# Kernel tuning notes

Measured on AMD Instinct MI355X. Metric: run time of the kernel, lower is better.

The kernel has to match this reference:

```python
import jax, jax.numpy as jnp
import numpy as np
import math
from jax import lax

C = 128
K = 9
PAD = K // 2


def conv1d(x, w, b):
    # x: [B, C, L], w: [C_out, C_in, K], b: [C_out]
    y = lax.conv_general_dilated(x, w, window_strides=(1,), padding=[(PAD, PAD)],
                                 dimension_numbers=('NCH', 'OIH', 'NCH'))
    return y + b[None, :, None]


def _scan_fwd(slices, w, b):
    # slices: [S, B, C, L]; recurrence s_i = s_i + relu(conv(s_{i-1})) for i=1..S-1
    def step(carry, s):
        new = s + jax.nn.relu(conv1d(carry, w, b))
        return new, new
    _, out = lax.scan(step, slices[0], slices[1:])
    return jnp.concatenate([slices[:1], out], axis=0)


def _scan_bwd(slices, w, b):
    # recurrence s_i = s_i + relu(conv(s_{i+1})) for i=S-2..1 (endpoints untouched)
    def step(carry, s):
        new = s + jax.nn.relu(conv1d(carry, w, b))
        return new, new
    seg = jnp.flip(slices[1:-1], axis=0)
    _, out = lax.scan(step, slices[-1], seg)
    return jnp.concatenate([slices[:1], jnp.flip(out, axis=0), slices[-1:]], axis=0)


def setup_inputs() -> dict:
    key = jax.random.key(0)
    ks = jax.random.split(key, 9)
    B, H, W = 64, 36, 100
    bound = math.sqrt(2.0 / (C * K * 5))
    bias_bound = 1.0 / math.sqrt(C * K)
    x = jax.random.normal(ks[0], (B, C, H, W), dtype=jnp.float32)
    def wgt(k):
        return jax.random.uniform(k, (C, C, K), dtype=jnp.float32, minval=-bound, maxval=bound)
    def bia(k):
        return jax.random.uniform(k, (C,), dtype=jnp.float32, minval=-bias_bound, maxval=bias_bound)
    return {
        'x': x,
        'w_d': wgt(ks[1]), 'b_d': bia(ks[2]),
        'w_u': wgt(ks[3]), 'b_u': bia(ks[4]),
        'w_r': wgt(ks[5]), 'b_r': bia(ks[6]),
        'w_l': wgt(ks[7]), 'b_l': bia(ks[8]),
    }


def reference(x, w_d, b_d, w_u, b_u, w_r, b_r, w_l, b_l):
    # Down then up passes: recurrence over H, 1D conv along W.
    rows = jnp.moveaxis(x, 2, 0)            # [H, B, C, W]
    rows = _scan_fwd(rows, w_d, b_d)
    rows = _scan_bwd(rows, w_u, b_u)
    y = jnp.moveaxis(rows, 0, 2)            # [B, C, H, W]
    # Right then left passes: recurrence over W, 1D conv along H.
    cols = jnp.moveaxis(y, 3, 0)            # [W, B, C, H]
    cols = _scan_fwd(cols, w_r, b_r)
    cols = _scan_bwd(cols, w_l, b_l)
    return jnp.moveaxis(cols, 0, 3)         # [B, C, H, W]
```

## Files before the change

kernel.cpp:

```cpp
#include <hip/hip_runtime.h>

#define B_ 64
#define C_ 128
#define H_ 36
#define W_ 100
#define K_ 9
#define PAD_ 4
#define NCHUNK 36
#define LDSTRIDE 152
#define NR_H 120
#define NR_W 56
#define PASSSZ (8 * NCHUNK * 64 * 8)
#define FBT_ELEMS ((size_t)B_ * W_ * C_ * H_)
#define FBT_OFF ((size_t)4 << 20)

typedef __attribute__((ext_vector_type(8))) short short8;
typedef __attribute__((ext_vector_type(4))) float f32x4;
typedef unsigned short u16;

__device__ __forceinline__ u16 f2bf(float f) {
    union { float f; unsigned u; } v; v.f = f;
    unsigned u = v.u;
    return (u16)((u + 0x7fffu + ((u >> 16) & 1u)) >> 16);
}
__device__ __forceinline__ float bf2f(u16 h) {
    union { unsigned u; float f; } v; v.u = ((unsigned)h) << 16; return v.f;
}
__device__ __forceinline__ float lodv(const float* p) { return *p; }
__device__ __forceinline__ float lodv(const u16* p) { return bf2f(*p); }
__device__ __forceinline__ void storv(float* p, float v) { *p = v; }
__device__ __forceinline__ void storv(u16* p, float v) { *p = f2bf(v); }

__global__ void prep_kernel(const float* __restrict__ wd, const float* __restrict__ wu,
                            const float* __restrict__ wr, const float* __restrict__ wl,
                            u16* __restrict__ afrag) {
    const int bid = blockIdx.x;
    const int p = bid / (8 * NCHUNK);
    const int rem = bid % (8 * NCHUNK);
    const int ct = rem / NCHUNK;
    const int kk = rem % NCHUNK;
    const float* w = (p == 0) ? wd : (p == 1) ? wu : (p == 2) ? wr : wl;
    const int lane = threadIdx.x;
    const int co = ct * 16 + (lane & 15);
    const int k0 = kk * 32 + ((lane >> 4) << 3);
    u16 v[8];
#pragma unroll
    for (int j = 0; j < 8; ++j) {
        const int k = k0 + j;
        const int kw = k >> 7;
        const int ci = k & 127;
        v[j] = f2bf(w[(co * C_ + ci) * K_ + kw]);
    }
    u16* dst = afrag + ((size_t)(bid * 64 + lane)) * 8;
#pragma unroll
    for (int j = 0; j < 8; ++j) dst[j] = v[j];
}

__device__ __forceinline__ void step_barrier() {
    asm volatile("s_waitcnt lgkmcnt(0)\n\ts_barrier" ::: "memory");
}

template <int AXIS, bool SKIP_T, bool STORE_T, int NROWS, typename TF>
__device__ __forceinline__ void run_pass(
    const float* __restrict__ stbase,
    const float* __restrict__ sread,
    float* __restrict__ fb,
    TF* __restrict__ fbT,
    const u16* __restrict__ afr,
    const float* __restrict__ bias,
    const int nsteps, const int start, const int dir, const int stage_t,
    u16* __restrict__ lds)
{
    constexpr int L = (AXIS == 0) ? W_ : H_;
    constexpr int NLT = (AXIS == 0) ? 7 : 3;
    const int tid = threadIdx.x;
    const int lane = tid & 63;
    const int wv = tid >> 6;
    const int q = lane >> 4, r = lane & 15;
    const int ct0 = 2 * wv, ct1 = ct0 + 1;
    const int cob0 = ct0 * 16 + (q << 2);
    const int cob1 = ct1 * 16 + (q << 2);

    short8 areg0[NCHUNK], areg1[NCHUNK];
    {
        const u16* ap0 = afr + ((size_t)(ct0 * NCHUNK) * 64 + lane) * 8;
        const u16* ap1 = afr + ((size_t)(ct1 * NCHUNK) * 64 + lane) * 8;
#pragma unroll
        for (int kk = 0; kk < NCHUNK; ++kk) {
            areg0[kk] = *(const short8*)(ap0 + (size_t)kk * 512);
            areg1[kk] = *(const short8*)(ap1 + (size_t)kk * 512);
            asm("" : "+a"(areg1[kk]));
            if (kk >= 18) asm("" : "+a"(areg0[kk]));
        }
    }
    float bias0[4], bias1[4];
#pragma unroll
    for (int j = 0; j < 4; ++j) { bias0[j] = bias[cob0 + j]; bias1[j] = bias[cob1 + j]; }

    __syncthreads();

    for (int e = tid; e < C_ * L; e += 256) {
        const int c = e / L, l = e - c * L;
        float fv;
        if constexpr (SKIP_T)
            fv = lodv(&fbT[((size_t)stage_t * C_ + c) * H_ + l]);
        else
            fv = stbase[(AXIS == 0) ? (c * H_ + stage_t) * W_ + l
                                    : (c * H_ + l) * W_ + stage_t];
        lds[(l + PAD_) * LDSTRIDE + c] = f2bf(fv);
        if constexpr (STORE_T && !SKIP_T)
            storv(&fbT[((size_t)stage_t * C_ + c) * H_ + l], fv);
    }
    __syncthreads();

    for (int s = 1; s <= nsteps; ++s) {
        const int cur = (s - 1) & 1, nxt = s & 1;
        const int t = start + dir * s;
        const u16* curb = lds + (size_t)cur * NROWS * LDSTRIDE;
        u16* nxtb = lds + (size_t)nxt * NROWS * LDSTRIDE;

#pragma unroll
        for (int ltp = 0; ltp < NLT; ltp += 2) {
            const bool two = (ltp + 1 < NLT);
            const int lA = ltp * 16 + r;
            const int lB = lA + 16;
            const bool vA = (lA < L);
            const bool vB = two && (lB < L);

            auto ld_skip = [&](int co, int l) -> float {
                if constexpr (SKIP_T) {
                    return lodv(&fbT[((size_t)t * C_ + co) * H_ + l]);
                } else {
                    const int fi = (AXIS == 0) ? (co * H_ + t) * W_ + l
                                               : (co * H_ + l) * W_ + t;
                    return sread[fi];
                }
            };
            float svA0[4], svA1[4], svB0[4], svB1[4];
#pragma unroll
            for (int j = 0; j < 4; ++j) {
                svA0[j] = vA ? ld_skip(cob0 + j, lA) : 0.0f;
                svA1[j] = vA ? ld_skip(cob1 + j, lA) : 0.0f;
                if (two) {
                    svB0[j] = vB ? ld_skip(cob0 + j, lB) : 0.0f;
                    svB1[j] = vB ? ld_skip(cob1 + j, lB) : 0.0f;
                }
            }

            f32x4 aA0 = {bias0[0], bias0[1], bias0[2], bias0[3]};
            f32x4 aA1 = {bias1[0], bias1[1], bias1[2], bias1[3]};
            f32x4 aB0 = aA0;
            f32x4 aB1 = aA1;
#pragma unroll
            for (int kk = 0; kk < NCHUNK; ++kk) {
                const int kw = kk >> 2;
                const int cib = ((kk & 3) << 5) | (q << 3);
                const short8 bvA = *(const short8*)&curb[(lA + kw) * LDSTRIDE + cib];
                aA0 = __builtin_amdgcn_mfma_f32_16x16x32_bf16(areg0[kk], bvA, aA0, 0, 0, 0);
                aA1 = __builtin_amdgcn_mfma_f32_16x16x32_bf16(areg1[kk], bvA, aA1, 0, 0, 0);
                if (two) {
                    const short8 bvB = *(const short8*)&curb[(lB + kw) * LDSTRIDE + cib];
                    aB0 = __builtin_amdgcn_mfma_f32_16x16x32_bf16(areg0[kk], bvB, aB0, 0, 0, 0);
                    aB1 = __builtin_amdgcn_mfma_f32_16x16x32_bf16(areg1[kk], bvB, aB1, 0, 0, 0);
                }
            }

            auto epi = [&](int l, bool valid, const f32x4& a, const float* sv,
                           const int cob) {
                if (!valid) return;
                union { u16 s4[4]; unsigned long long v; } pk;
#pragma unroll
                for (int j = 0; j < 4; ++j) {
                    const float conv = fmaxf(a[j], 0.0f);
                    const float nv = sv[j] + conv;
                    if constexpr (STORE_T) {
                        storv(&fbT[((size_t)t * C_ + cob + j) * H_ + l], nv);
                    } else {
                        const int fi = (AXIS == 0) ? ((cob + j) * H_ + t) * W_ + l
                                                   : ((cob + j) * H_ + l) * W_ + t;
                        fb[fi] = nv;
                    }
                    pk.s4[j] = f2bf(nv);
                }
                *(unsigned long long*)&nxtb[(l + PAD_) * LDSTRIDE + cob] = pk.v;
            };
            epi(lA, vA, aA0, svA0, cob0);
            epi(lA, vA, aA1, svA1, cob1);
            if (two) {
                epi(lB, vB, aB0, svB0, cob0);
                epi(lB, vB, aB1, svB1, cob1);
            }
        }
        step_barrier();
    }
}

__global__ __launch_bounds__(256, 1) void spatialH(
    const float* __restrict__ x, float* __restrict__ fb,
    const u16* __restrict__ afrag,
    const float* __restrict__ bd, const float* __restrict__ bu) {
    __shared__ __align__(16) u16 lds[2 * NR_H * LDSTRIDE];
    const int b = blockIdx.x;
    const int tid = threadIdx.x;
    const float* xb = x + (size_t)b * C_ * H_ * W_;
    float* fbb = fb + (size_t)b * C_ * H_ * W_;

    for (int e = tid; e < C_ * W_; e += 256) {
        const int c = e / W_, w = e - c * W_;
        fbb[(c * H_) * W_ + w] = xb[(c * H_) * W_ + w];
    }
    for (int off = tid * 8; off < 2 * NR_H * LDSTRIDE; off += 256 * 8)
        *(uint4*)(&lds[off]) = make_uint4(0u, 0u, 0u, 0u);

    run_pass<0, false, false, NR_H, float>(xb, xb, fbb, (float*)nullptr,
        afrag + (size_t)0 * PASSSZ, bd, 35, 0, +1, 0, lds);
    run_pass<0, false, false, NR_H, float>(fbb, fbb, fbb, (float*)nullptr,
        afrag + (size_t)1 * PASSSZ, bu, 34, 35, -1, 35, lds);
}

template <typename TF>
__global__ void t1_kernel(const float* __restrict__ in, TF* __restrict__ fbT) {
    __shared__ float tile[16 * 36 * 17];
    const int tid = threadIdx.x;
    const int bid = blockIdx.x;
    const int b = bid / 56;
    const int rem = bid % 56;
    const int cs = rem / 7, wc = rem % 7;
    const int w0 = wc * 16;
    const int wlen = (w0 + 16 <= W_) ? 16 : (W_ - w0);
    const int c0 = cs * 16;
    const float* src = in + (size_t)b * C_ * H_ * W_;
    TF* dst = fbT + (size_t)b * W_ * C_ * H_;

    for (int j = tid; j < 576 * 16; j += 256) {
        const int w = j & 15;
        const int ch = j >> 4;
        if (w >= wlen) continue;
        const int c = ch / 36, h = ch - c * 36;
        tile[(c * 36 + h) * 17 + w] = src[((size_t)(c0 + c) * H_ + h) * W_ + w0 + w];
    }
    __syncthreads();
    for (int i = tid; i < 576 * wlen; i += 256) {
        const int w = i / 576;
        const int ch = i - w * 576;
        const int c = ch / 36, h = ch - c * 36;
        storv(&dst[((size_t)(w0 + w) * C_ + c0 + c) * H_ + h],
              tile[(c * 36 + h) * 17 + w]);
    }
}

template <typename TF>
__global__ __launch_bounds__(256, 1) void spatialW(
    TF* __restrict__ fbT, const u16* __restrict__ afrag,
    const float* __restrict__ br_, const float* __restrict__ bl_) {
    __shared__ __align__(16) u16 lds[2 * NR_W * LDSTRIDE];
    const int b = blockIdx.x;
    const int tid = threadIdx.x;
    TF* fbTb = fbT + (size_t)b * W_ * C_ * H_;

    for (int off = tid * 8; off < 2 * NR_W * LDSTRIDE; off += 256 * 8)
        *(uint4*)(&lds[off]) = make_uint4(0u, 0u, 0u, 0u);

    run_pass<1, true, true, NR_W, TF>((const float*)nullptr, (const float*)nullptr,
        (float*)nullptr, fbTb, afrag + (size_t)2 * PASSSZ, br_, 99, 0, +1, 0, lds);
    run_pass<1, true, true, NR_W, TF>((const float*)nullptr, (const float*)nullptr,
        (float*)nullptr, fbTb, afrag + (size_t)3 * PASSSZ, bl_, 98, 99, -1, 99, lds);
}

template <typename TF>
__global__ void t2_kernel(const TF* __restrict__ fbT, float* __restrict__ out) {
    __shared__ float tile[16 * 36 * 17];
    const int tid = threadIdx.x;
    const int bid = blockIdx.x;
    const int b = bid / 56;
    const int rem = bid % 56;
    const int cs = rem / 7, wc = rem % 7;
    const int w0 = wc * 16;
    const int wlen = (w0 + 16 <= W_) ? 16 : (W_ - w0);
    const int c0 = cs * 16;
    const TF* src = fbT + (size_t)b * W_ * C_ * H_;

    for (int i = tid; i < 576 * wlen; i += 256) {
        const int w = i / 576;
        const int ch = i - w * 576;
        const int c = ch / 36, h = ch - c * 36;
        tile[(c * 36 + h) * 17 + w] = lodv(&src[((size_t)(w0 + w) * C_ + c0 + c) * H_ + h]);
    }
    __syncthreads();
    for (int j = tid; j < 576 * 16; j += 256) {
        const int w = j & 15;
        const int ch = j >> 4;
        if (w >= wlen) continue;
        const int c = ch / 36, h = ch - c * 36;
        out[(((size_t)b * C_ + c0 + c) * H_ + h) * W_ + w0 + w] = tile[(c * 36 + h) * 17 + w];
    }
}

extern "C" void kernel_launch(void* const* d_in, const int* in_sizes, int n_in,
                              void* d_out, int out_size, void* d_ws, size_t ws_size,
                              hipStream_t stream) {
    const float* x  = (const float*)d_in[0];
    const float* wd = (const float*)d_in[1];
    const float* bd = (const float*)d_in[2];
    const float* wu = (const float*)d_in[3];
    const float* bu = (const float*)d_in[4];
    const float* wr = (const float*)d_in[5];
    const float* br = (const float*)d_in[6];
    const float* wl = (const float*)d_in[7];
    const float* bl = (const float*)d_in[8];

    u16* afrag = (u16*)((char*)d_ws + 1024);
    void* fbTp = (char*)d_ws + FBT_OFF;
    const bool f32ok = ws_size >= FBT_OFF + sizeof(float) * FBT_ELEMS;

    prep_kernel<<<dim3(4 * 8 * NCHUNK), dim3(64), 0, stream>>>(wd, wu, wr, wl, afrag);
    spatialH<<<dim3(64), dim3(256), 0, stream>>>(x, (float*)d_out, afrag, bd, bu);
    if (f32ok) {
        t1_kernel<float><<<dim3(64 * 56), dim3(256), 0, stream>>>(
            (const float*)d_out, (float*)fbTp);
        spatialW<float><<<dim3(64), dim3(256), 0, stream>>>(
            (float*)fbTp, afrag, br, bl);
        t2_kernel<float><<<dim3(64 * 56), dim3(256), 0, stream>>>(
            (const float*)fbTp, (float*)d_out);
    } else {
        t1_kernel<u16><<<dim3(64 * 56), dim3(256), 0, stream>>>(
            (const float*)d_out, (u16*)fbTp);
        spatialW<u16><<<dim3(64), dim3(256), 0, stream>>>(
            (u16*)fbTp, afrag, br, bl);
        t2_kernel<u16><<<dim3(64 * 56), dim3(256), 0, stream>>>(
            (const u16*)fbTp, (float*)d_out);
    }
}
```

Measured before the change: 1.465 ms.

## Reuse LDS B-fragments across conv taps via DPP lane shifts

The step loop is restructured so every L-tile's B fragment is loaded from LDS once per channel quarter, and later kernel taps are produced by DPP row shifts across lanes that pull in the next tile's data, instead of issuing a separate LDS read for each of the nine taps. All L-tiles' accumulators are kept live together, and the skip loads are hoisted ahead of the MMA loop. This cuts LDS read traffic by roughly nine times but raises VGPR pressure, so more A fragments are pinned to AGPRs. The DPP row_shr with bound_ctrl and the OR-merge of the neighbour tile must reproduce the padded window exactly at the 16-lane row edges.

```diff
diff --git a/kernel.cpp b/kernel.cpp
--- a/kernel.cpp
+++ b/kernel.cpp
@@ -16,7 +16,10 @@
 
 typedef __attribute__((ext_vector_type(8))) short short8;
 typedef __attribute__((ext_vector_type(4))) float f32x4;
+typedef __attribute__((ext_vector_type(4))) int i32x4;
 typedef unsigned short u16;
+
+union fragU { short8 s; i32x4 i; };
 
 __device__ __forceinline__ u16 f2bf(float f) {
     union { float f; unsigned u; } v; v.f = f;
@@ -30,6 +33,22 @@
 __device__ __forceinline__ float lodv(const u16* p) { return bf2f(*p); }
 __device__ __forceinline__ void storv(float* p, float v) { *p = v; }
 __device__ __forceinline__ void storv(u16* p, float v) { *p = f2bf(v); }
+
+__device__ __forceinline__ i32x4 dpp_shift(i32x4 cur, i32x4 nxt) {
+    i32x4 o;
+#pragma unroll
+    for (int j = 0; j < 4; ++j)
+        o[j] = __builtin_amdgcn_update_dpp(0, cur[j], 0x101, 0xF, 0xF, false)
+             | __builtin_amdgcn_update_dpp(0, nxt[j], 0x11F, 0xF, 0xF, false);
+    return o;
+}
+__device__ __forceinline__ i32x4 dpp_shift_last(i32x4 cur) {
+    i32x4 o;
+#pragma unroll
+    for (int j = 0; j < 4; ++j)
+        o[j] = __builtin_amdgcn_update_dpp(0, cur[j], 0x101, 0xF, 0xF, false);
+    return o;
+}
 
 __global__ void prep_kernel(const float* __restrict__ wd, const float* __restrict__ wu,
                             const float* __restrict__ wr, const float* __restrict__ wl,
@@ -90,7 +109,7 @@
             areg0[kk] = *(const short8*)(ap0 + (size_t)kk * 512);
             areg1[kk] = *(const short8*)(ap1 + (size_t)kk * 512);
             asm("" : "+a"(areg1[kk]));
-            if (kk >= 18) asm("" : "+a"(areg0[kk]));
+            if (kk >= 9) asm("" : "+a"(areg0[kk]));
         }
     }
     float bias0[4], bias1[4];
@@ -119,76 +138,82 @@
         const u16* curb = lds + (size_t)cur * NROWS * LDSTRIDE;
         u16* nxtb = lds + (size_t)nxt * NROWS * LDSTRIDE;
 
-#pragma unroll
-        for (int ltp = 0; ltp < NLT; ltp += 2) {
-            const bool two = (ltp + 1 < NLT);
-            const int lA = ltp * 16 + r;
-            const int lB = lA + 16;
-            const bool vA = (lA < L);
-            const bool vB = two && (lB < L);
-
-            auto ld_skip = [&](int co, int l) -> float {
-                if constexpr (SKIP_T) {
-                    return lodv(&fbT[((size_t)t * C_ + co) * H_ + l]);
+        auto ld_skip = [&](int co, int l) -> float {
+            if constexpr (SKIP_T) {
+                return lodv(&fbT[((size_t)t * C_ + co) * H_ + l]);
+            } else {
+                const int fi = (AXIS == 0) ? (co * H_ + t) * W_ + l
+                                           : (co * H_ + l) * W_ + t;
+                return sread[fi];
+            }
+        };
+
+        float sv0[NLT][4], sv1[NLT][4];
+#pragma unroll
+        for (int lt = 0; lt < NLT; ++lt) {
+            const int l = lt * 16 + r;
+            const bool v = (l < L);
+#pragma unroll
+            for (int j = 0; j < 4; ++j) {
+                sv0[lt][j] = v ? ld_skip(cob0 + j, l) : 0.0f;
+                sv1[lt][j] = v ? ld_skip(cob1 + j, l) : 0.0f;
+            }
+        }
+
+        f32x4 acc0[NLT], acc1[NLT];
+#pragma unroll
+        for (int lt = 0; lt < NLT; ++lt) {
+            acc0[lt] = f32x4{bias0[0], bias0[1], bias0[2], bias0[3]};
+            acc1[lt] = f32x4{bias1[0], bias1[1], bias1[2], bias1[3]};
+        }
+
+#pragma unroll
+        for (int cq = 0; cq < 4; ++cq) {
+            i32x4 frag[NLT];
+#pragma unroll
+            for (int lt = 0; lt < NLT; ++lt)
+                frag[lt] = *(const i32x4*)&curb[(lt * 16 + r) * LDSTRIDE + (cq << 5) + (q << 3)];
+#pragma unroll
+            for (int kw = 0; kw < 9; ++kw) {
+                const int kk = kw * 4 + cq;
+#pragma unroll
+                for (int lt = 0; lt < NLT; ++lt) {
+                    fragU u; u.i = frag[lt];
+                    acc0[lt] = __builtin_amdgcn_mfma_f32_16x16x32_bf16(areg0[kk], u.s, acc0[lt], 0, 0, 0);
+                    acc1[lt] = __builtin_amdgcn_mfma_f32_16x16x32_bf16(areg1[kk], u.s, acc1[lt], 0, 0, 0);
+                }
+                if (kw < 8) {
+#pragma unroll
+                    for (int lt = 0; lt < NLT; ++lt)
+                        frag[lt] = (lt + 1 < NLT) ? dpp_shift(frag[lt], frag[lt + 1])
+                                                  : dpp_shift_last(frag[lt]);
+                }
+            }
+        }
+
+        auto epi = [&](int l, const f32x4& a, const float* sv, const int cob) {
+            union { u16 s4[4]; unsigned long long v; } pk;
+#pragma unroll
+            for (int j = 0; j < 4; ++j) {
+                const float conv = fmaxf(a[j], 0.0f);
+                const float nv = sv[j] + conv;
+                if constexpr (STORE_T) {
+                    storv(&fbT[((size_t)t * C_ + cob + j) * H_ + l], nv);
                 } else {
-                    const int fi = (AXIS == 0) ? (co * H_ + t) * W_ + l
-                                               : (co * H_ + l) * W_ + t;
-                    return sread[fi];
+                    const int fi = (AXIS == 0) ? ((cob + j) * H_ + t) * W_ + l
+                                               : ((cob + j) * H_ + l) * W_ + t;
+                    fb[fi] = nv;
                 }
-            };
-            float svA0[4], svA1[4], svB0[4], svB1[4];
-#pragma unroll
-            for (int j = 0; j < 4; ++j) {
-                svA0[j] = vA ? ld_skip(cob0 + j, lA) : 0.0f;
-                svA1[j] = vA ? ld_skip(cob1 + j, lA) : 0.0f;
-                if (two) {
-                    svB0[j] = vB ? ld_skip(cob0 + j, lB) : 0.0f;
-                    svB1[j] = vB ? ld_skip(cob1 + j, lB) : 0.0f;
-                }
-            }
-
-            f32x4 aA0 = {bias0[0], bias0[1], bias0[2], bias0[3]};
-            f32x4 aA1 = {bias1[0], bias1[1], bias1[2], bias1[3]};
-            f32x4 aB0 = aA0;
-            f32x4 aB1 = aA1;
-#pragma unroll
-            for (int kk = 0; kk < NCHUNK; ++kk) {
-                const int kw = kk >> 2;
-                const int cib = ((kk & 3) << 5) | (q << 3);
-                const short8 bvA = *(const short8*)&curb[(lA + kw) * LDSTRIDE + cib];
-                aA0 = __builtin_amdgcn_mfma_f32_16x16x32_bf16(areg0[kk], bvA, aA0, 0, 0, 0);
-                aA1 = __builtin_amdgcn_mfma_f32_16x16x32_bf16(areg1[kk], bvA, aA1, 0, 0, 0);
-                if (two) {
-                    const short8 bvB = *(const short8*)&curb[(lB + kw) * LDSTRIDE + cib];
-                    aB0 = __builtin_amdgcn_mfma_f32_16x16x32_bf16(areg0[kk], bvB, aB0, 0, 0, 0);
-                    aB1 = __builtin_amdgcn_mfma_f32_16x16x32_bf16(areg1[kk], bvB, aB1, 0, 0, 0);
-                }
-            }
-
-            auto epi = [&](int l, bool valid, const f32x4& a, const float* sv,
-                           const int cob) {
-                if (!valid) return;
-                union { u16 s4[4]; unsigned long long v; } pk;
-#pragma unroll
-                for (int j = 0; j < 4; ++j) {
-                    const float conv = fmaxf(a[j], 0.0f);
-                    const float nv = sv[j] + conv;
-                    if constexpr (STORE_T) {
-                        storv(&fbT[((size_t)t * C_ + cob + j) * H_ + l], nv);
-                    } else {
-                        const int fi = (AXIS == 0) ? ((cob + j) * H_ + t) * W_ + l
-                                                   : ((cob + j) * H_ + l) * W_ + t;
-                        fb[fi] = nv;
-                    }
-                    pk.s4[j] = f2bf(nv);
-                }
-                *(unsigned long long*)&nxtb[(l + PAD_) * LDSTRIDE + cob] = pk.v;
-            };
-            epi(lA, vA, aA0, svA0, cob0);
-            epi(lA, vA, aA1, svA1, cob1);
-            if (two) {
-                epi(lB, vB, aB0, svB0, cob0);
-                epi(lB, vB, aB1, svB1, cob1);
+                pk.s4[j] = f2bf(nv);
+            }
+            *(unsigned long long*)&nxtb[(l + PAD_) * LDSTRIDE + cob] = pk.v;
+        };
+#pragma unroll
+        for (int lt = 0; lt < NLT; ++lt) {
+            const int l = lt * 16 + r;
+            if (l < L) {
+                epi(l, acc0[lt], sv0[lt], cob0);
+                epi(l, acc1[lt], sv1[lt], cob1);
             }
         }
         step_barrier();
```

Measured after the change: 1.788 ms. 22.1% more time.
